# Kernel tuning notes

Measured on AMD Instinct MI355X. Metric: run time of the kernel, lower is better.

The kernel has to match this reference:

```python
import jax, jax.numpy as jnp
import numpy as np

B, T = 8, 1024
C_IN, C_H = 4096, 4096
K_I, K_H = 3, 3
INIT_SPARSITY = 0.15


def _fixed_fanin_bipartite(rng, n_out, n_in, k):
    # exactly k True entries per row, distinct columns
    r = rng.random((n_out, n_in))
    cols = np.argsort(r, axis=1)[:, :k]
    A = np.zeros((n_out, n_in), np.float32)
    np.put_along_axis(A, cols, 1.0, axis=1)
    return A


def _fixed_fanin_graph(rng, n, k):
    # exactly k True entries per row, distinct non-self columns
    r = rng.random((n, n))
    np.fill_diagonal(r, 2.0)  # exclude self-loops
    cols = np.argsort(r, axis=1)[:, :k]
    A = np.zeros((n, n), np.float32)
    np.put_along_axis(A, cols, 1.0, axis=1)
    return A


def setup_inputs() -> dict:
    rng = np.random.default_rng(0)
    z = jnp.asarray(rng.random((B, T, C_IN)) < INIT_SPARSITY)          # bool (B,T,C_in)
    h0 = jnp.asarray(rng.random((B, C_H)) < INIT_SPARSITY)             # bool (B,C_h)
    A_input_f = jnp.asarray(_fixed_fanin_bipartite(rng, C_H, C_IN, K_I))  # (C_h,C_in) f32
    A_hidden_f = jnp.asarray(_fixed_fanin_graph(rng, C_H, K_H))           # (C_h,C_h) f32
    return {"z": z, "h0": h0, "A_input_f": A_input_f, "A_hidden_f": A_hidden_f}


def reference(z, h0, A_input_f, A_hidden_f):
    # AND-of-ORs CA: h_i(t) = [OR over input fan-in of z(t)] AND [OR over hidden fan-in of h(t-1)]
    z_tf = jnp.moveaxis(z, -2, 0)  # (T, B, C_in)

    def step(h, z_t):
        input_or = (z_t.astype(jnp.float32) @ A_input_f.T) > 0   # (B, C_h) bool
        hidden_or = (h.astype(jnp.float32) @ A_hidden_f.T) > 0   # (B, C_h) bool
        h_new = input_or & hidden_or
        return h_new, h_new

    _, h_seq = jax.lax.scan(step, h0, z_tf)   # (T, B, C_h)
    h_seq = jnp.moveaxis(h_seq, 0, -2)        # (B, T, C_h)
    return jnp.concatenate([z, h_seq], axis=-1)  # (B, T, C_in + C_h) bool
```

## Files before the change

### kernel.cpp

```cpp
#include <hip/hip_runtime.h>
#include <stdint.h>

#define B_   8
#define T_   1024
#define CIN_ 4096
#define CH_  4096


__device__ __forceinline__ uint32_t bytes_nonzero01(uint32_t w) {
  uint32_t t = (w & 0x7F7F7F7Fu) + 0x7F7F7F7Fu;
  t = (t | w) & 0x80808080u;
  return t >> 7;
}

__device__ __forceinline__ uint32_t load4(const void* base, long idx4, int es) {
  if (es == 1) {
    uint32_t w = ((const uint32_t*)base)[idx4];
    return bytes_nonzero01(w);
  } else if (es == 2) {
    uint32_t w0 = ((const uint32_t*)base)[idx4 * 2];
    uint32_t w1 = ((const uint32_t*)base)[idx4 * 2 + 1];
    uint32_t r = 0;
    r |= ((w0 & 0xFFFFu) != 0u) ? 0x00000001u : 0u;
    r |= ((w0 >> 16)     != 0u) ? 0x00000100u : 0u;
    r |= ((w1 & 0xFFFFu) != 0u) ? 0x00010000u : 0u;
    r |= ((w1 >> 16)     != 0u) ? 0x01000000u : 0u;
    return r;
  } else {
    uint4 w = ((const uint4*)base)[idx4];
    uint32_t r = 0;
    r |= (w.x != 0u) ? 0x00000001u : 0u;
    r |= (w.y != 0u) ? 0x00000100u : 0u;
    r |= (w.z != 0u) ? 0x00010000u : 0u;
    r |= (w.w != 0u) ? 0x01000000u : 0u;
    return r;
  }
}

__device__ __forceinline__ uint4 expand01(uint32_t v4) {
  uint4 r = { v4 & 1u, (v4 >> 8) & 1u, (v4 >> 16) & 1u, (v4 >> 24) & 1u };
  return r;
}

__global__ __launch_bounds__(256) void extract_kernel(const float* __restrict__ Ain,
                                                      const float* __restrict__ Ah,
                                                      uint32_t* __restrict__ idxin,
                                                      uint32_t* __restrict__ idxh,
                                                      const uint32_t* __restrict__ z,
                                                      uint32_t* __restrict__ modep) {
  if (blockIdx.x == 2048) {
    __shared__ int sB, sH, sW, sL;
    const int n = threadIdx.x;
    if (n == 0) { sB = 1; sH = 1; sW = 1; sL = 0; }
    __syncthreads();
    int okB = 1, okH = 1, okW = 1, low = 0;
    for (int k = 0; k < 16; ++k) {
      uint32_t w = z[n + 256 * k];
      if ((w & 0xFEFEFEFEu) != 0u) okB = 0;
      uint32_t lo = w & 0xFFFFu, hi = w >> 16;
      if (!((lo == 0u || lo == 0x3F80u) && (hi == 0u || hi == 0x3F80u))) okH = 0;
      if (!(w == 0u || w == 1u)) okW = 0;
      if (lo != 0u) low = 1;
    }
    if (!okB) atomicAnd(&sB, 0);
    if (!okH) atomicAnd(&sH, 0);
    if (!okW) atomicAnd(&sW, 0);
    if (low)  atomicOr(&sL, 1);
    __syncthreads();
    if (n == 0) {
      uint32_t mode;
      if (sW)      mode = 4;
      else if (sB) mode = 1;
      else if (sH) mode = sL ? 2 : 4;
      else         mode = 1;
      modep[0] = mode;
    }
    return;
  }
  const int wave = threadIdx.x >> 6;
  const int lane = threadIdx.x & 63;
  const int row  = blockIdx.x * 4 + wave;
  const float* A;
  uint32_t* outp;
  if (row < 4096) { A = Ain + (long)row * 4096;          outp = idxin + row * 3; }
  else            { A = Ah  + (long)(row - 4096) * 4096; outp = idxh + (row - 4096) * 3; }
  __shared__ int cnt[4];
  if (lane == 0) cnt[wave] = 0;
  __syncthreads();
  const float4* A4 = (const float4*)A;
  #pragma unroll
  for (int it = 0; it < 16; ++it) {
    float4 v = A4[it * 64 + lane];
    int cbase = (it * 64 + lane) * 4;
    if (v.x != 0.0f) { int p = atomicAdd(&cnt[wave], 1); if (p < 3) outp[p] = cbase;     }
    if (v.y != 0.0f) { int p = atomicAdd(&cnt[wave], 1); if (p < 3) outp[p] = cbase + 1; }
    if (v.z != 0.0f) { int p = atomicAdd(&cnt[wave], 1); if (p < 3) outp[p] = cbase + 2; }
    if (v.w != 0.0f) { int p = atomicAdd(&cnt[wave], 1); if (p < 3) outp[p] = cbase + 3; }
  }
}

__global__ __launch_bounds__(1024) void inor_kernel(const void* __restrict__ z,
                                                    const uint32_t* __restrict__ idxin,
                                                    const uint32_t* __restrict__ modep,
                                                    uint32_t* __restrict__ in_orb,
                                                    uint32_t* __restrict__ out) {
  const int t = blockIdx.x;
  const int n = threadIdx.x;
  const int es = (int)modep[0];
  __shared__ __align__(16) unsigned char zp[4096];
  uint32_t acc = 0;
  #pragma unroll
  for (int b = 0; b < B_; ++b) {
    uint32_t v4 = load4(z, ((long)b * T_ + t) * 1024 + n, es);
    acc |= v4 << b;
    ((uint4*)(out + ((long)b * T_ + t) * 8192))[n] = expand01(v4);
  }
  ((uint32_t*)zp)[n] = acc;
  __syncthreads();
  const uint4* ip = (const uint4*)(idxin + n * 12);
  uint4 q0 = ip[0], q1 = ip[1], q2 = ip[2];
  uint32_t r0 = (uint32_t)zp[q0.x] | zp[q0.y] | zp[q0.z];
  uint32_t r1 = (uint32_t)zp[q0.w] | zp[q1.x] | zp[q1.y];
  uint32_t r2 = (uint32_t)zp[q1.z] | zp[q1.w] | zp[q2.x];
  uint32_t r3 = (uint32_t)zp[q2.y] | zp[q2.z] | zp[q2.w];
  in_orb[t * 1024 + n] = r0 | (r1 << 8) | (r2 << 16) | (r3 << 24);
}

__global__ __launch_bounds__(1024) void scan_kernel(const uint32_t* __restrict__ in_orb,
                                                    const uint32_t* __restrict__ idxh,
                                                    const void* __restrict__ h0,
                                                    const uint32_t* __restrict__ modep,
                                                    uint32_t* __restrict__ out) {
  const int b = blockIdx.x;
  const int n = threadIdx.x;
  const int es = (int)modep[0];
  __shared__ __align__(16) unsigned char hbuf[2][4096];

  uint32_t d[4][3];
  {
    const uint4* p = (const uint4*)(idxh + n * 12);
    uint4 q0 = p[0], q1 = p[1], q2 = p[2];
    d[0][0] = q0.x; d[0][1] = q0.y; d[0][2] = q0.z;
    d[1][0] = q0.w; d[1][1] = q1.x; d[1][2] = q1.y;
    d[2][0] = q1.z; d[2][1] = q1.w; d[2][2] = q2.x;
    d[3][0] = q2.y; d[3][1] = q2.z; d[3][2] = q2.w;
  }

  ((uint32_t*)hbuf[0])[n] = load4(h0, (long)b * 1024 + n, es);
  __syncthreads();

  uint32_t* outh = out + (long)b * T_ * 8192 + 4096;

  int p = 0;
  uint32_t inw = in_orb[n];
  for (int t = 0; t < T_; ++t) {
    uint32_t inw_next = (t + 1 < T_) ? in_orb[(t + 1) * 1024 + n] : 0u;
    const unsigned char* hc = &hbuf[p][0];
    unsigned char* hn = &hbuf[p ^ 1][0];

    uint32_t mask = (inw >> b) & 0x01010101u;
    uint32_t out4 = 0;
    if (mask) {
      if (mask & 0x00000001u) {
        uint32_t v = (uint32_t)hc[d[0][0]] | hc[d[0][1]] | hc[d[0][2]];
        out4 |= v;
      }
      if (mask & 0x00000100u) {
        uint32_t v = (uint32_t)hc[d[1][0]] | hc[d[1][1]] | hc[d[1][2]];
        out4 |= v << 8;
      }
      if (mask & 0x00010000u) {
        uint32_t v = (uint32_t)hc[d[2][0]] | hc[d[2][1]] | hc[d[2][2]];
        out4 |= v << 16;
      }
      if (mask & 0x01000000u) {
        uint32_t v = (uint32_t)hc[d[3][0]] | hc[d[3][1]] | hc[d[3][2]];
        out4 |= v << 24;
      }
    }
    ((uint32_t*)hn)[n] = out4;
    ((uint4*)(outh + (long)t * 8192))[n] = expand01(out4);
    __syncthreads();

    inw = inw_next;
    p ^= 1;
  }
}

extern "C" void kernel_launch(void* const* d_in, const int* in_sizes, int n_in,
                              void* d_out, int out_size, void* d_ws, size_t ws_size,
                              hipStream_t stream) {
  const void*  z   = d_in[0];
  const void*  h0  = d_in[1];
  const float* Ain = (const float*)d_in[2];
  const float* Ah  = (const float*)d_in[3];
  uint32_t* out = (uint32_t*)d_out;

  char* ws = (char*)d_ws;
  uint32_t* modep = (uint32_t*)(ws);
  uint32_t* idxin = (uint32_t*)(ws + 256);
  uint32_t* idxh  = (uint32_t*)(ws + 256 + 49152);
  uint32_t* inorb = (uint32_t*)(ws + 98560);

  extract_kernel<<<2049, 256,  0, stream>>>(Ain, Ah, idxin, idxh,
                                            (const uint32_t*)z, modep);
  inor_kernel   <<<T_,   1024, 0, stream>>>(z, idxin, modep, inorb, out);
  scan_kernel   <<<B_,   1024, 0, stream>>>(inorb, idxh, h0, modep, out);
}
```

Before: 951.9 us.

## Precompute bank-conflict-aware gather schedule for hidden fan-in and unroll scan by two

```diff
diff --git a/kernel.cpp b/kernel.cpp
--- a/kernel.cpp
+++ b/kernel.cpp
@@ -101,13 +101,66 @@
 
 __global__ __launch_bounds__(1024) void inor_kernel(const void* __restrict__ z,
                                                     const uint32_t* __restrict__ idxin,
+                                                    const uint32_t* __restrict__ idxh,
                                                     const uint32_t* __restrict__ modep,
                                                     uint32_t* __restrict__ in_orb,
                                                     uint32_t* __restrict__ out) {
+  __shared__ __align__(16) unsigned char zp[4096];
+  __shared__ uint16_t cnt[16][12][32];
+
+  if (blockIdx.x == T_) {
+    const int n  = threadIdx.x;
+    const int wv = n >> 6, ln = n & 63;
+    const uint4* p = (const uint4*)(idxh + n * 12);
+    uint4 q0 = p[0], q1 = p[1], q2 = p[2];
+    uint32_t d[12] = { q0.x, q0.y, q0.z,  q0.w, q1.x, q1.y,
+                       q1.z, q1.w, q2.x,  q2.y, q2.z, q2.w };
+    for (int i = threadIdx.x; i < 16 * 12 * 32; i += 1024) ((uint16_t*)cnt)[i] = 0;
+    __syncthreads();
+    int slotOf[12];
+    uint32_t freem = 0xFFFu;
+    for (int l = 0; l < 64; ++l) {
+      if (ln == l) {
+        #pragma unroll
+        for (int e = 0; e < 12; ++e) {
+          uint32_t bank = (d[e] >> 2) & 31u;
+          int best = 0; uint32_t bc = 0xFFFFFFFFu;
+          #pragma unroll
+          for (int k = 0; k < 12; ++k) {
+            if ((freem >> k) & 1u) {
+              uint32_t c = cnt[wv][k][bank];
+              if (c < bc) { bc = c; best = k; }
+            }
+          }
+          slotOf[e] = best;
+          freem &= ~(1u << best);
+          cnt[wv][best][bank] = (uint16_t)(cnt[wv][best][bank] + 1);
+        }
+      }
+    }
+    __syncthreads();
+    uint32_t wv6[6]; uint32_t S = 0;
+    #pragma unroll
+    for (int k = 0; k < 12; ++k) {
+      uint32_t de = 0, je = 0;
+      #pragma unroll
+      for (int e = 0; e < 12; ++e) {
+        bool m = (slotOf[e] == k);
+        de = m ? d[e] : de;
+        je = m ? (uint32_t)(e / 3) : je;
+      }
+      if (k & 1) wv6[k >> 1] |= de << 16; else wv6[k >> 1] = de;
+      S |= je << (2 * k);
+    }
+    uint4* o4 = (uint4*)((uint32_t*)idxh + (size_t)n * 8);
+    o4[0] = make_uint4(wv6[0], wv6[1], wv6[2], wv6[3]);
+    o4[1] = make_uint4(wv6[4], wv6[5], S, 0u);
+    return;
+  }
+
   const int t = blockIdx.x;
   const int n = threadIdx.x;
   const int es = (int)modep[0];
-  __shared__ __align__(16) unsigned char zp[4096];
   uint32_t acc = 0;
   #pragma unroll
   for (int b = 0; b < B_; ++b) {
@@ -127,63 +180,51 @@
 }
 
 __global__ __launch_bounds__(1024) void scan_kernel(const uint32_t* __restrict__ in_orb,
-                                                    const uint32_t* __restrict__ idxh,
+                                                    const uint32_t* __restrict__ sched,
                                                     const void* __restrict__ h0,
                                                     const uint32_t* __restrict__ modep,
                                                     uint32_t* __restrict__ out) {
   const int b = blockIdx.x;
   const int n = threadIdx.x;
   const int es = (int)modep[0];
-  __shared__ __align__(16) unsigned char hbuf[2][4096];
-
-  uint32_t d[4][3];
-  {
-    const uint4* p = (const uint4*)(idxh + n * 12);
-    uint4 q0 = p[0], q1 = p[1], q2 = p[2];
-    d[0][0] = q0.x; d[0][1] = q0.y; d[0][2] = q0.z;
-    d[1][0] = q0.w; d[1][1] = q1.x; d[1][2] = q1.y;
-    d[2][0] = q1.z; d[2][1] = q1.w; d[2][2] = q2.x;
-    d[3][0] = q2.y; d[3][1] = q2.z; d[3][2] = q2.w;
-  }
-
-  ((uint32_t*)hbuf[0])[n] = load4(h0, (long)b * 1024 + n, es);
+  __shared__ __align__(128) unsigned char hbuf[2][4096];
+
+  const uint4* sp = (const uint4*)(sched + (size_t)n * 8);
+  uint4 s0 = sp[0], s1 = sp[1];
+  uint32_t aw[6] = { s0.x, s0.y, s0.z, s0.w, s1.x, s1.y };
+  uint32_t aA[12], aB[12], sh[12];
+  #pragma unroll
+  for (int e = 0; e < 12; ++e) {
+    uint32_t a = (aw[e >> 1] >> ((e & 1) * 16)) & 0xFFFFu;
+    aA[e] = a; aB[e] = a + 4096u;
+    sh[e] = ((s1.z >> (2 * e)) & 3u) * 8u;
+  }
+
+  unsigned char* lds8 = &hbuf[0][0];
+  ((uint32_t*)lds8)[n] = load4(h0, (long)b * 1024 + n, es);
   __syncthreads();
 
   uint32_t* outh = out + (long)b * T_ * 8192 + 4096;
 
-  int p = 0;
-  uint32_t inw = in_orb[n];
-  for (int t = 0; t < T_; ++t) {
-    uint32_t inw_next = (t + 1 < T_) ? in_orb[(t + 1) * 1024 + n] : 0u;
-    const unsigned char* hc = &hbuf[p][0];
-    unsigned char* hn = &hbuf[p ^ 1][0];
-
-    uint32_t mask = (inw >> b) & 0x01010101u;
-    uint32_t out4 = 0;
-    if (mask) {
-      if (mask & 0x00000001u) {
-        uint32_t v = (uint32_t)hc[d[0][0]] | hc[d[0][1]] | hc[d[0][2]];
-        out4 |= v;
-      }
-      if (mask & 0x00000100u) {
-        uint32_t v = (uint32_t)hc[d[1][0]] | hc[d[1][1]] | hc[d[1][2]];
-        out4 |= v << 8;
-      }
-      if (mask & 0x00010000u) {
-        uint32_t v = (uint32_t)hc[d[2][0]] | hc[d[2][1]] | hc[d[2][2]];
-        out4 |= v << 16;
-      }
-      if (mask & 0x01000000u) {
-        uint32_t v = (uint32_t)hc[d[3][0]] | hc[d[3][1]] | hc[d[3][2]];
-        out4 |= v << 24;
-      }
-    }
-    ((uint32_t*)hn)[n] = out4;
-    ((uint4*)(outh + (long)t * 8192))[n] = expand01(out4);
-    __syncthreads();
-
-    inw = inw_next;
-    p ^= 1;
+  uint32_t inw0 = in_orb[n];
+  for (int t = 0; t < T_; t += 2) {
+    uint32_t inw1 = in_orb[(t + 1) * 1024 + n];
+    uint32_t o = 0;
+    #pragma unroll
+    for (int e = 0; e < 12; ++e) o |= ((uint32_t)lds8[aA[e]]) << sh[e];
+    o &= (inw0 >> b) & 0x01010101u;
+    ((uint32_t*)(lds8 + 4096))[n] = o;
+    ((uint4*)(outh + (long)t * 8192))[n] = expand01(o);
+    __syncthreads();
+    uint32_t inw2 = (t + 2 < T_) ? in_orb[(t + 2) * 1024 + n] : 0u;
+    uint32_t o2 = 0;
+    #pragma unroll
+    for (int e = 0; e < 12; ++e) o2 |= ((uint32_t)lds8[aB[e]]) << sh[e];
+    o2 &= (inw1 >> b) & 0x01010101u;
+    ((uint32_t*)lds8)[n] = o2;
+    ((uint4*)(outh + (long)(t + 1) * 8192))[n] = expand01(o2);
+    __syncthreads();
+    inw0 = inw2;
   }
 }
 
@@ -201,9 +242,10 @@
   uint32_t* idxin = (uint32_t*)(ws + 256);
   uint32_t* idxh  = (uint32_t*)(ws + 256 + 49152);
   uint32_t* inorb = (uint32_t*)(ws + 98560);
+  uint32_t* sched = idxh;
 
   extract_kernel<<<2049, 256,  0, stream>>>(Ain, Ah, idxin, idxh,
                                             (const uint32_t*)z, modep);
-  inor_kernel   <<<T_,   1024, 0, stream>>>(z, idxin, modep, inorb, out);
-  scan_kernel   <<<B_,   1024, 0, stream>>>(inorb, idxh, h0, modep, out);
-}
+  inor_kernel   <<<T_ + 1, 1024, 0, stream>>>(z, idxin, idxh, modep, inorb, out);
+  scan_kernel   <<<B_,   1024, 0, stream>>>(inorb, sched, h0, modep, out);
+}
```

Result: slower. 1.356 ms (+42.5%).

## Compact active neuron records per step to shorten the serial hidden-state scan

Applied to the files above, without the earlier changes.

```diff
diff --git a/kernel.cpp b/kernel.cpp
--- a/kernel.cpp
+++ b/kernel.cpp
@@ -5,6 +5,7 @@
 #define T_   1024
 #define CIN_ 4096
 #define CH_  4096
+#define RCAP 1920
 
 
 __device__ __forceinline__ uint32_t bytes_nonzero01(uint32_t w) {
@@ -101,13 +102,19 @@
 
 __global__ __launch_bounds__(1024) void inor_kernel(const void* __restrict__ z,
                                                     const uint32_t* __restrict__ idxin,
+                                                    const uint32_t* __restrict__ idxh,
                                                     const uint32_t* __restrict__ modep,
                                                     uint32_t* __restrict__ in_orb,
-                                                    uint32_t* __restrict__ out) {
+                                                    uint32_t* __restrict__ out,
+                                                    uint2* __restrict__ recs,
+                                                    uint32_t* __restrict__ actcnt) {
   const int t = blockIdx.x;
   const int n = threadIdx.x;
+  const int lane = n & 63, wv = n >> 6;
   const int es = (int)modep[0];
   __shared__ __align__(16) unsigned char zp[4096];
+  __shared__ uint32_t wsum[B_][16];
+
   uint32_t acc = 0;
   #pragma unroll
   for (int b = 0; b < B_; ++b) {
@@ -123,7 +130,102 @@
   uint32_t r1 = (uint32_t)zp[q0.w] | zp[q1.x] | zp[q1.y];
   uint32_t r2 = (uint32_t)zp[q1.z] | zp[q1.w] | zp[q2.x];
   uint32_t r3 = (uint32_t)zp[q2.y] | zp[q2.z] | zp[q2.w];
-  in_orb[t * 1024 + n] = r0 | (r1 << 8) | (r2 << 16) | (r3 << 24);
+  uint32_t w = r0 | (r1 << 8) | (r2 << 16) | (r3 << 24);
+  in_orb[t * 1024 + n] = w;
+
+  if (recs == nullptr) return;
+
+  const uint4* hp = (const uint4*)(idxh + n * 12);
+  uint4 h0q = hp[0], h1q = hp[1], h2q = hp[2];
+  const uint32_t s00 = h0q.x, s01 = h0q.y, s02 = h0q.z;
+  const uint32_t s10 = h0q.w, s11 = h1q.x, s12 = h1q.y;
+  const uint32_t s20 = h1q.z, s21 = h1q.w, s22 = h2q.x;
+  const uint32_t s30 = h2q.y, s31 = h2q.z, s32 = h2q.w;
+
+  uint32_t mB[B_], exB[B_];
+  const uint64_t ltm = (1ull << lane) - 1ull;
+  #pragma unroll
+  for (int b = 0; b < B_; ++b) {
+    uint32_t m = (w >> b) & 0x01010101u;
+    mB[b] = m;
+    uint32_t ex = 0, tot = 0;
+    #pragma unroll
+    for (int j = 0; j < 4; ++j) {
+      uint64_t bl = __ballot((m >> (8 * j)) & 1u);
+      ex  += (uint32_t)__popcll(bl & ltm);
+      tot += (uint32_t)__popcll(bl);
+    }
+    exB[b] = ex;
+    if (lane == 0) wsum[b][wv] = tot;
+  }
+  __syncthreads();
+  #pragma unroll
+  for (int b = 0; b < B_; ++b) {
+    uint32_t base = exB[b];
+    for (int wq = 0; wq < wv; ++wq) base += wsum[b][wq];
+    uint2* rb = recs + ((size_t)b * T_ + t) * RCAP;
+    uint32_t m = mB[b];
+    uint32_t pos = base;
+    if (m & 0x00000001u) { if (pos < RCAP) rb[pos] = make_uint2((uint32_t)(4*n+0) | (s00 << 16), s01 | (s02 << 16)); pos++; }
+    if (m & 0x00000100u) { if (pos < RCAP) rb[pos] = make_uint2((uint32_t)(4*n+1) | (s10 << 16), s11 | (s12 << 16)); pos++; }
+    if (m & 0x00010000u) { if (pos < RCAP) rb[pos] = make_uint2((uint32_t)(4*n+2) | (s20 << 16), s21 | (s22 << 16)); pos++; }
+    if (m & 0x01000000u) { if (pos < RCAP) rb[pos] = make_uint2((uint32_t)(4*n+3) | (s30 << 16), s31 | (s32 << 16)); pos++; }
+  }
+  if (n == 0) {
+    #pragma unroll
+    for (int b = 0; b < B_; ++b) {
+      uint32_t tot = 0;
+      for (int wq = 0; wq < 16; ++wq) tot += wsum[b][wq];
+      actcnt[b * T_ + t] = tot;
+    }
+  }
+}
+
+__global__ __launch_bounds__(1024) void scan_compact(const uint2* __restrict__ recs,
+                                                     const uint32_t* __restrict__ actcnt,
+                                                     const void* __restrict__ h0,
+                                                     const uint32_t* __restrict__ modep,
+                                                     uint32_t* __restrict__ out) {
+  const int b = blockIdx.x;
+  const int n = threadIdx.x;
+  const int es = (int)modep[0];
+  __shared__ __align__(16) unsigned char hb[3][4096];
+
+  ((uint32_t*)hb[0])[n] = load4(h0, (long)b * 1024 + n, es);
+  ((uint32_t*)hb[1])[n] = 0u;
+
+  const uint2* recB = recs + (size_t)b * T_ * RCAP;
+  uint32_t* outh = out + (long)b * T_ * 8192 + 4096;
+
+  uint32_t cnt = min(actcnt[b * T_], (uint32_t)RCAP);
+  uint4 pf = make_uint4(0, 0, 0, 0);
+  if ((uint32_t)(2 * n) < cnt) pf = ((const uint4*)recB)[n];
+  __syncthreads();
+
+  for (int t = 0; t < T_; ++t) {
+    const int rd = t % 3, wr = (t + 1) % 3, cl = (t + 2) % 3;
+    const unsigned char* hc = hb[rd];
+    unsigned char* hn = hb[wr];
+    uint4 rec = pf;
+    const uint32_t c = cnt;
+    if (t + 1 < T_) {
+      cnt = min(actcnt[b * T_ + t + 1], (uint32_t)RCAP);
+      if ((uint32_t)(2 * n) < cnt)
+        pf = ((const uint4*)(recB + (size_t)(t + 1) * RCAP))[n];
+    }
+    if (n < 256) ((uint4*)hb[cl])[n] = make_uint4(0, 0, 0, 0);
+    if ((uint32_t)(2 * n) < c) {
+      uint32_t v = (uint32_t)hc[rec.x >> 16] | hc[rec.y & 0xFFFFu] | hc[rec.y >> 16];
+      hn[rec.x & 0xFFFFu] = (unsigned char)v;
+    }
+    if ((uint32_t)(2 * n + 1) < c) {
+      uint32_t v = (uint32_t)hc[rec.z >> 16] | hc[rec.w & 0xFFFFu] | hc[rec.w >> 16];
+      hn[rec.z & 0xFFFFu] = (unsigned char)v;
+    }
+    if (t > 0) ((uint4*)(outh + (long)(t - 1) * 8192))[n] = expand01(((const uint32_t*)hc)[n]);
+    __syncthreads();
+  }
+  ((uint4*)(outh + (long)(T_ - 1) * 8192))[n] = expand01(((const uint32_t*)hb[T_ % 3])[n]);
 }
 
 __global__ __launch_bounds__(1024) void scan_kernel(const uint32_t* __restrict__ in_orb,
@@ -145,43 +247,26 @@
     d[2][0] = q1.z; d[2][1] = q1.w; d[2][2] = q2.x;
     d[3][0] = q2.y; d[3][1] = q2.z; d[3][2] = q2.w;
   }
-
   ((uint32_t*)hbuf[0])[n] = load4(h0, (long)b * 1024 + n, es);
   __syncthreads();
-
   uint32_t* outh = out + (long)b * T_ * 8192 + 4096;
-
   int p = 0;
   uint32_t inw = in_orb[n];
   for (int t = 0; t < T_; ++t) {
     uint32_t inw_next = (t + 1 < T_) ? in_orb[(t + 1) * 1024 + n] : 0u;
     const unsigned char* hc = &hbuf[p][0];
     unsigned char* hn = &hbuf[p ^ 1][0];
-
     uint32_t mask = (inw >> b) & 0x01010101u;
     uint32_t out4 = 0;
     if (mask) {
-      if (mask & 0x00000001u) {
-        uint32_t v = (uint32_t)hc[d[0][0]] | hc[d[0][1]] | hc[d[0][2]];
-        out4 |= v;
-      }
-      if (mask & 0x00000100u) {
-        uint32_t v = (uint32_t)hc[d[1][0]] | hc[d[1][1]] | hc[d[1][2]];
-        out4 |= v << 8;
-      }
-      if (mask & 0x00010000u) {
-        uint32_t v = (uint32_t)hc[d[2][0]] | hc[d[2][1]] | hc[d[2][2]];
-        out4 |= v << 16;
-      }
-      if (mask & 0x01000000u) {
-        uint32_t v = (uint32_t)hc[d[3][0]] | hc[d[3][1]] | hc[d[3][2]];
-        out4 |= v << 24;
-      }
+      if (mask & 0x00000001u) { uint32_t v = (uint32_t)hc[d[0][0]] | hc[d[0][1]] | hc[d[0][2]]; out4 |= v; }
+      if (mask & 0x00000100u) { uint32_t v = (uint32_t)hc[d[1][0]] | hc[d[1][1]] | hc[d[1][2]]; out4 |= v << 8; }
+      if (mask & 0x00010000u) { uint32_t v = (uint32_t)hc[d[2][0]] | hc[d[2][1]] | hc[d[2][2]]; out4 |= v << 16; }
+      if (mask & 0x01000000u) { uint32_t v = (uint32_t)hc[d[3][0]] | hc[d[3][1]] | hc[d[3][2]]; out4 |= v << 24; }
     }
     ((uint32_t*)hn)[n] = out4;
     ((uint4*)(outh + (long)t * 8192))[n] = expand01(out4);
     __syncthreads();
-
     inw = inw_next;
     p ^= 1;
   }
@@ -201,9 +286,18 @@
   uint32_t* idxin = (uint32_t*)(ws + 256);
   uint32_t* idxh  = (uint32_t*)(ws + 256 + 49152);
   uint32_t* inorb = (uint32_t*)(ws + 98560);
-
-  extract_kernel<<<2049, 256,  0, stream>>>(Ain, Ah, idxin, idxh,
-                                            (const uint32_t*)z, modep);
-  inor_kernel   <<<T_,   1024, 0, stream>>>(z, idxin, modep, inorb, out);
-  scan_kernel   <<<B_,   1024, 0, stream>>>(inorb, idxh, h0, modep, out);
-}
+  uint32_t* actc  = (uint32_t*)(ws + 4292864);
+  uint2*    recs  = (uint2*)   (ws + 4325632);
+
+  const size_t need = 4325632 + (size_t)B_ * T_ * RCAP * sizeof(uint2);
+  const bool compact = (ws_size >= need);
+
+  extract_kernel<<<2048 + 1, 256, 0, stream>>>(Ain, Ah, idxin, idxh,
+                                               (const uint32_t*)z, modep);
+  inor_kernel<<<T_, 1024, 0, stream>>>(z, idxin, idxh, modep, inorb, out,
+                                       compact ? recs : nullptr, actc);
+  if (compact)
+    scan_compact<<<B_, 1024, 0, stream>>>(recs, actc, h0, modep, out);
+  else
+    scan_kernel<<<B_, 1024, 0, stream>>>(inorb, idxh, h0, modep, out);
+}
```

After: 1.141 ms. 1.2x slower.

## Fuse extract, input-OR and scan into one persistent kernel with flag-based sync

Applied to the files above, without the earlier changes.

```diff
diff --git a/kernel.cpp b/kernel.cpp
--- a/kernel.cpp
+++ b/kernel.cpp
@@ -42,148 +42,162 @@
   return r;
 }
 
-__global__ __launch_bounds__(256) void extract_kernel(const float* __restrict__ Ain,
-                                                      const float* __restrict__ Ah,
-                                                      uint32_t* __restrict__ idxin,
-                                                      uint32_t* __restrict__ idxh,
-                                                      const uint32_t* __restrict__ z,
-                                                      uint32_t* __restrict__ modep) {
-  if (blockIdx.x == 2048) {
-    __shared__ int sB, sH, sW, sL;
-    const int n = threadIdx.x;
-    if (n == 0) { sB = 1; sH = 1; sW = 1; sL = 0; }
-    __syncthreads();
-    int okB = 1, okH = 1, okW = 1, low = 0;
-    for (int k = 0; k < 16; ++k) {
-      uint32_t w = z[n + 256 * k];
-      if ((w & 0xFEFEFEFEu) != 0u) okB = 0;
-      uint32_t lo = w & 0xFFFFu, hi = w >> 16;
-      if (!((lo == 0u || lo == 0x3F80u) && (hi == 0u || hi == 0x3F80u))) okH = 0;
-      if (!(w == 0u || w == 1u)) okW = 0;
-      if (lo != 0u) low = 1;
-    }
-    if (!okB) atomicAnd(&sB, 0);
-    if (!okH) atomicAnd(&sH, 0);
-    if (!okW) atomicAnd(&sW, 0);
-    if (low)  atomicOr(&sL, 1);
+__device__ __forceinline__ void wait_ge(uint32_t* p, uint32_t tgt) {
+  while (__hip_atomic_load(p, __ATOMIC_RELAXED, __HIP_MEMORY_SCOPE_AGENT) < tgt)
+    __builtin_amdgcn_s_sleep(16);
+  __threadfence();
+}
+__device__ __forceinline__ void bump(uint32_t* p) {
+  __threadfence();
+  __hip_atomic_fetch_add(p, 1u, __ATOMIC_RELAXED, __HIP_MEMORY_SCOPE_AGENT);
+}
+
+#define BID_DETECT 8
+#define BID_EXT0   9
+#define BID_INOR0  521
+#define NBLK       (521 + T_)
+
+__global__ __launch_bounds__(1024) void mega_kernel(const void* __restrict__ z,
+                                                    const void* __restrict__ h0,
+                                                    const float* __restrict__ Ain,
+                                                    const float* __restrict__ Ah,
+                                                    uint32_t* __restrict__ modep,
+                                                    uint32_t* __restrict__ idxin,
+                                                    uint32_t* __restrict__ idxh,
+                                                    uint32_t* __restrict__ inorb,
+                                                    uint32_t* __restrict__ flags,
+                                                    uint32_t* __restrict__ out) {
+  __shared__ __align__(16) unsigned char sm[2][4096];
+  __shared__ int cnt[16];
+  const int bid = blockIdx.x;
+  const int n = threadIdx.x;
+
+  if (bid < 8) {
+    const int b = bid;
+    if (n == 0) { wait_ge(&flags[0], 1); wait_ge(&flags[2], 256); }
+    __syncthreads();
+    const int es = (int)modep[0];
+    uint32_t d[4][3];
+    {
+      const uint4* p = (const uint4*)(idxh + n * 12);
+      uint4 q0 = p[0], q1 = p[1], q2 = p[2];
+      d[0][0] = q0.x; d[0][1] = q0.y; d[0][2] = q0.z;
+      d[1][0] = q0.w; d[1][1] = q1.x; d[1][2] = q1.y;
+      d[2][0] = q1.z; d[2][1] = q1.w; d[2][2] = q2.x;
+      d[3][0] = q2.y; d[3][1] = q2.z; d[3][2] = q2.w;
+    }
+    ((uint32_t*)sm[0])[n] = load4(h0, (long)b * 1024 + n, es);
+    __syncthreads();
+    uint32_t* outh = out + (long)b * T_ * 8192 + 4096;
+    int p = 0;
+    for (int g = 0; g < 32; ++g) {
+      if (n == 0) wait_ge(&flags[8 + g], 32);
+      __syncthreads();
+      uint32_t inw = inorb[(g * 32) * 1024 + n];
+      for (int tt = 0; tt < 32; ++tt) {
+        const int t = g * 32 + tt;
+        uint32_t inw_next = (tt < 31) ? inorb[(t + 1) * 1024 + n] : 0u;
+        const unsigned char* hc = &sm[p][0];
+        unsigned char* hn = &sm[p ^ 1][0];
+        uint32_t mask = (inw >> b) & 0x01010101u;
+        uint32_t o4 = 0;
+        if (mask) {
+          if (mask & 0x00000001u) { uint32_t v = (uint32_t)hc[d[0][0]] | hc[d[0][1]] | hc[d[0][2]]; o4 |= v; }
+          if (mask & 0x00000100u) { uint32_t v = (uint32_t)hc[d[1][0]] | hc[d[1][1]] | hc[d[1][2]]; o4 |= v << 8; }
+          if (mask & 0x00010000u) { uint32_t v = (uint32_t)hc[d[2][0]] | hc[d[2][1]] | hc[d[2][2]]; o4 |= v << 16; }
+          if (mask & 0x01000000u) { uint32_t v = (uint32_t)hc[d[3][0]] | hc[d[3][1]] | hc[d[3][2]]; o4 |= v << 24; }
+        }
+        ((uint32_t*)hn)[n] = o4;
+        ((uint4*)(outh + (long)t * 8192))[n] = expand01(o4);
+        __syncthreads();
+        inw = inw_next;
+        p ^= 1;
+      }
+    }
+    return;
+  }
+
+  if (bid == BID_DETECT) {
+    if (n == 0) { cnt[0] = 1; cnt[1] = 1; cnt[2] = 1; cnt[3] = 0; }
+    __syncthreads();
+    if (n < 256) {
+      const uint32_t* zw = (const uint32_t*)z;
+      int okB = 1, okH = 1, okW = 1, low = 0;
+      for (int k = 0; k < 16; ++k) {
+        uint32_t w = zw[n + 256 * k];
+        if ((w & 0xFEFEFEFEu) != 0u) okB = 0;
+        uint32_t lo = w & 0xFFFFu, hi = w >> 16;
+        if (!((lo == 0u || lo == 0x3F80u) && (hi == 0u || hi == 0x3F80u))) okH = 0;
+        if (!(w == 0u || w == 1u)) okW = 0;
+        if (lo != 0u) low = 1;
+      }
+      if (!okB) atomicAnd(&cnt[0], 0);
+      if (!okH) atomicAnd(&cnt[1], 0);
+      if (!okW) atomicAnd(&cnt[2], 0);
+      if (low)  atomicOr(&cnt[3], 1);
+    }
     __syncthreads();
     if (n == 0) {
       uint32_t mode;
-      if (sW)      mode = 4;
-      else if (sB) mode = 1;
-      else if (sH) mode = sL ? 2 : 4;
-      else         mode = 1;
+      if (cnt[2])      mode = 4;
+      else if (cnt[0]) mode = 1;
+      else if (cnt[1]) mode = cnt[3] ? 2 : 4;
+      else             mode = 1;
       modep[0] = mode;
-    }
-    return;
-  }
-  const int wave = threadIdx.x >> 6;
-  const int lane = threadIdx.x & 63;
-  const int row  = blockIdx.x * 4 + wave;
-  const float* A;
-  uint32_t* outp;
-  if (row < 4096) { A = Ain + (long)row * 4096;          outp = idxin + row * 3; }
-  else            { A = Ah  + (long)(row - 4096) * 4096; outp = idxh + (row - 4096) * 3; }
-  __shared__ int cnt[4];
-  if (lane == 0) cnt[wave] = 0;
-  __syncthreads();
-  const float4* A4 = (const float4*)A;
-  #pragma unroll
-  for (int it = 0; it < 16; ++it) {
-    float4 v = A4[it * 64 + lane];
-    int cbase = (it * 64 + lane) * 4;
-    if (v.x != 0.0f) { int p = atomicAdd(&cnt[wave], 1); if (p < 3) outp[p] = cbase;     }
-    if (v.y != 0.0f) { int p = atomicAdd(&cnt[wave], 1); if (p < 3) outp[p] = cbase + 1; }
-    if (v.z != 0.0f) { int p = atomicAdd(&cnt[wave], 1); if (p < 3) outp[p] = cbase + 2; }
-    if (v.w != 0.0f) { int p = atomicAdd(&cnt[wave], 1); if (p < 3) outp[p] = cbase + 3; }
-  }
-}
-
-__global__ __launch_bounds__(1024) void inor_kernel(const void* __restrict__ z,
-                                                    const uint32_t* __restrict__ idxin,
-                                                    const uint32_t* __restrict__ modep,
-                                                    uint32_t* __restrict__ in_orb,
-                                                    uint32_t* __restrict__ out) {
-  const int t = blockIdx.x;
-  const int n = threadIdx.x;
-  const int es = (int)modep[0];
-  __shared__ __align__(16) unsigned char zp[4096];
-  uint32_t acc = 0;
-  #pragma unroll
-  for (int b = 0; b < B_; ++b) {
-    uint32_t v4 = load4(z, ((long)b * T_ + t) * 1024 + n, es);
-    acc |= v4 << b;
-    ((uint4*)(out + ((long)b * T_ + t) * 8192))[n] = expand01(v4);
-  }
-  ((uint32_t*)zp)[n] = acc;
-  __syncthreads();
-  const uint4* ip = (const uint4*)(idxin + n * 12);
-  uint4 q0 = ip[0], q1 = ip[1], q2 = ip[2];
-  uint32_t r0 = (uint32_t)zp[q0.x] | zp[q0.y] | zp[q0.z];
-  uint32_t r1 = (uint32_t)zp[q0.w] | zp[q1.x] | zp[q1.y];
-  uint32_t r2 = (uint32_t)zp[q1.z] | zp[q1.w] | zp[q2.x];
-  uint32_t r3 = (uint32_t)zp[q2.y] | zp[q2.z] | zp[q2.w];
-  in_orb[t * 1024 + n] = r0 | (r1 << 8) | (r2 << 16) | (r3 << 24);
-}
-
-__global__ __launch_bounds__(1024) void scan_kernel(const uint32_t* __restrict__ in_orb,
-                                                    const uint32_t* __restrict__ idxh,
-                                                    const void* __restrict__ h0,
-                                                    const uint32_t* __restrict__ modep,
-                                                    uint32_t* __restrict__ out) {
-  const int b = blockIdx.x;
-  const int n = threadIdx.x;
-  const int es = (int)modep[0];
-  __shared__ __align__(16) unsigned char hbuf[2][4096];
-
-  uint32_t d[4][3];
+      bump(&flags[0]);
+    }
+    return;
+  }
+
+  if (bid < BID_INOR0) {
+    const int eb = bid - BID_EXT0;
+    const int wave = n >> 6, lane = n & 63;
+    const int isH = (eb < 256);
+    const int row = (isH ? eb : eb - 256) * 16 + wave;
+    const float* A = (isH ? Ah : Ain) + (long)row * 4096;
+    uint32_t* outp = (isH ? idxh : idxin) + row * 3;
+    if (lane == 0) cnt[wave] = 0;
+    __syncthreads();
+    const float4* A4 = (const float4*)A;
+    #pragma unroll
+    for (int it = 0; it < 16; ++it) {
+      float4 v = A4[it * 64 + lane];
+      int cbase = (it * 64 + lane) * 4;
+      if (v.x != 0.0f) { int q = atomicAdd(&cnt[wave], 1); if (q < 3) outp[q] = cbase;     }
+      if (v.y != 0.0f) { int q = atomicAdd(&cnt[wave], 1); if (q < 3) outp[q] = cbase + 1; }
+      if (v.z != 0.0f) { int q = atomicAdd(&cnt[wave], 1); if (q < 3) outp[q] = cbase + 2; }
+      if (v.w != 0.0f) { int q = atomicAdd(&cnt[wave], 1); if (q < 3) outp[q] = cbase + 3; }
+    }
+    __syncthreads();
+    if (n == 0) bump(isH ? &flags[2] : &flags[1]);
+    return;
+  }
+
   {
-    const uint4* p = (const uint4*)(idxh + n * 12);
-    uint4 q0 = p[0], q1 = p[1], q2 = p[2];
-    d[0][0] = q0.x; d[0][1] = q0.y; d[0][2] = q0.z;
-    d[1][0] = q0.w; d[1][1] = q1.x; d[1][2] = q1.y;
-    d[2][0] = q1.z; d[2][1] = q1.w; d[2][2] = q2.x;
-    d[3][0] = q2.y; d[3][1] = q2.z; d[3][2] = q2.w;
-  }
-
-  ((uint32_t*)hbuf[0])[n] = load4(h0, (long)b * 1024 + n, es);
-  __syncthreads();
-
-  uint32_t* outh = out + (long)b * T_ * 8192 + 4096;
-
-  int p = 0;
-  uint32_t inw = in_orb[n];
-  for (int t = 0; t < T_; ++t) {
-    uint32_t inw_next = (t + 1 < T_) ? in_orb[(t + 1) * 1024 + n] : 0u;
-    const unsigned char* hc = &hbuf[p][0];
-    unsigned char* hn = &hbuf[p ^ 1][0];
-
-    uint32_t mask = (inw >> b) & 0x01010101u;
-    uint32_t out4 = 0;
-    if (mask) {
-      if (mask & 0x00000001u) {
-        uint32_t v = (uint32_t)hc[d[0][0]] | hc[d[0][1]] | hc[d[0][2]];
-        out4 |= v;
-      }
-      if (mask & 0x00000100u) {
-        uint32_t v = (uint32_t)hc[d[1][0]] | hc[d[1][1]] | hc[d[1][2]];
-        out4 |= v << 8;
-      }
-      if (mask & 0x00010000u) {
-        uint32_t v = (uint32_t)hc[d[2][0]] | hc[d[2][1]] | hc[d[2][2]];
-        out4 |= v << 16;
-      }
-      if (mask & 0x01000000u) {
-        uint32_t v = (uint32_t)hc[d[3][0]] | hc[d[3][1]] | hc[d[3][2]];
-        out4 |= v << 24;
-      }
-    }
-    ((uint32_t*)hn)[n] = out4;
-    ((uint4*)(outh + (long)t * 8192))[n] = expand01(out4);
-    __syncthreads();
-
-    inw = inw_next;
-    p ^= 1;
+    const int t = bid - BID_INOR0;
+    if (n == 0) { wait_ge(&flags[0], 1); wait_ge(&flags[1], 256); }
+    __syncthreads();
+    const int es = (int)modep[0];
+    uint32_t acc = 0;
+    #pragma unroll
+    for (int b = 0; b < B_; ++b) {
+      uint32_t v4 = load4(z, ((long)b * T_ + t) * 1024 + n, es);
+      acc |= v4 << b;
+      ((uint4*)(out + ((long)b * T_ + t) * 8192))[n] = expand01(v4);
+    }
+    ((uint32_t*)sm[0])[n] = acc;
+    __syncthreads();
+    const unsigned char* zp = &sm[0][0];
+    const uint4* ip = (const uint4*)(idxin + n * 12);
+    uint4 q0 = ip[0], q1 = ip[1], q2 = ip[2];
+    uint32_t r0 = (uint32_t)zp[q0.x] | zp[q0.y] | zp[q0.z];
+    uint32_t r1 = (uint32_t)zp[q0.w] | zp[q1.x] | zp[q1.y];
+    uint32_t r2 = (uint32_t)zp[q1.z] | zp[q1.w] | zp[q2.x];
+    uint32_t r3 = (uint32_t)zp[q2.y] | zp[q2.z] | zp[q2.w];
+    inorb[t * 1024 + n] = r0 | (r1 << 8) | (r2 << 16) | (r3 << 24);
+    __syncthreads();
+    if (n == 0) bump(&flags[8 + (t >> 5)]);
+    return;
   }
 }
 
@@ -201,9 +215,9 @@
   uint32_t* idxin = (uint32_t*)(ws + 256);
   uint32_t* idxh  = (uint32_t*)(ws + 256 + 49152);
   uint32_t* inorb = (uint32_t*)(ws + 98560);
-
-  extract_kernel<<<2049, 256,  0, stream>>>(Ain, Ah, idxin, idxh,
-                                            (const uint32_t*)z, modep);
-  inor_kernel   <<<T_,   1024, 0, stream>>>(z, idxin, modep, inorb, out);
-  scan_kernel   <<<B_,   1024, 0, stream>>>(inorb, idxh, h0, modep, out);
-}
+  uint32_t* flagp = (uint32_t*)(ws + 4292864);
+
+  hipMemsetAsync(flagp, 0, 4096, stream);
+  mega_kernel<<<NBLK, 1024, 0, stream>>>(z, h0, Ain, Ah, modep, idxin, idxh,
+                                         inorb, flagp, out);
+}
```

New measurement: 1.131 ms. +18.8%, slower.
